# Performance work log

Measured on AMD Instinct MI355X. Metric: run time of the kernel, lower is better.

## Reference

```python
import jax, jax.numpy as jnp
import numpy as np

B, N, C = 4, 4096, 512
C8 = C // 8

def setup_inputs() -> dict:
    key = jax.random.key(0)
    ks = jax.random.split(key, 4)
    x = jax.random.normal(ks[0], (B, N, C), dtype=jnp.float32)
    # 1x1 Conv1D kernels == dense matmuls over channel dim
    Wf = jax.random.normal(ks[1], (C, C8), dtype=jnp.float32) * 0.02
    bf = jnp.zeros((C8,), dtype=jnp.float32)
    Wg = jax.random.normal(ks[2], (C, C8), dtype=jnp.float32) * 0.02
    bg = jnp.zeros((C8,), dtype=jnp.float32)
    Wh = jax.random.normal(ks[3], (C, C), dtype=jnp.float32) * 0.02
    bh = jnp.zeros((C,), dtype=jnp.float32)
    gamma = jnp.float32(1.0)  # learned scalar (zero-init in original; nonzero to exercise path)
    return {"x": x, "Wf": Wf, "bf": bf, "Wg": Wg, "bg": bg, "Wh": Wh, "bh": bh, "gamma": gamma}

def reference(x, Wf, bf, Wg, bg, Wh, bh, gamma):
    # 1x1 conv projections (kernel_size=1 -> per-position matmul)
    f_x = jnp.einsum('bnc,cd->bnd', x, Wf) + bf          # [B, N, C/8]
    g_x = jnp.einsum('bnc,cd->bnd', x, Wg) + bg          # [B, N, C/8]
    h_x = jnp.einsum('bnc,cd->bnd', x, Wh) + bh          # [B, N, C]
    # unscaled single-head attention: softmax(f g^T) h
    scores = jnp.einsum('bnd,bmd->bnm', f_x, g_x)        # [B, N, N]
    attn = jax.nn.softmax(scores, axis=-1)
    out = jnp.einsum('bnm,bmd->bnd', attn, h_x)          # [B, N, C]
    return x + gamma * out
```

## Files before the change

kernel.cpp:

```cpp
#include <hip/hip_runtime.h>
#include <stdint.h>

typedef uint16_t u16;
typedef __attribute__((ext_vector_type(8))) __bf16    bf16x8;
typedef __attribute__((ext_vector_type(4))) __bf16    bf16x4;
typedef __attribute__((ext_vector_type(8))) uint16_t  u16x8;
typedef __attribute__((ext_vector_type(4))) uint16_t  u16x4;
typedef __attribute__((ext_vector_type(4))) float     f32x4;

#define LOG2E 1.44269504088896340736f
#define MFMA16(a, b, c) __builtin_amdgcn_mfma_f32_16x16x32_bf16((a), (b), (c), 0, 0, 0)

__device__ __forceinline__ u16 f2b(float f) {
  uint32_t u = __builtin_bit_cast(uint32_t, f);
  u += 0x7fffu + ((u >> 16) & 1u);
  return (u16)(u >> 16);
}

__device__ __forceinline__ bf16x8 ldsFrag(const u16* base, int row, int chunk) {
  const u16* p = base + row * 64 + ((chunk ^ (row & 7)) << 3);
  u16x8 raw = *(const u16x8*)p;
  return __builtin_bit_cast(bf16x8, raw);
}
__device__ __forceinline__ void ldsPut(u16* base, int row, int logicalChunk, u16x8 v) {
  u16* p = base + row * 64 + ((logicalChunk ^ (row & 7)) << 3);
  *(u16x8*)p = v;
}

__device__ __forceinline__ void dma16(const u16* g, u16* l) {
  __builtin_amdgcn_global_load_lds(
      (const __attribute__((address_space(1))) uint32_t*)g,
      (__attribute__((address_space(3))) uint32_t*)l, 16, 0, 0);
}

__global__ __launch_bounds__(256) void pack_weights2(
    const float* __restrict__ Wf, const float* __restrict__ Wg,
    const float* __restrict__ Wh, const float* __restrict__ bfv,
    const float* __restrict__ bgv, const float* __restrict__ bhv,
    u16* __restrict__ Wt, float* __restrict__ biasc) {
  __shared__ u16 T[64 * 64];
  const int nt = blockIdx.x >> 3;
  const int kt = blockIdx.x & 7;
  const int n0 = nt * 64, k0 = kt * 64;
  const float* src; int stride, cbase; float scale = 1.0f;
  if (nt == 0)      { src = Wf; stride = 64;  cbase = 0;        scale = LOG2E; }
  else if (nt == 1) { src = Wg; stride = 64;  cbase = 0; }
  else              { src = Wh; stride = 512; cbase = n0 - 128; }
  const int t = threadIdx.x;
  const int cl = (t & 15) * 4, r0 = t >> 4;
#pragma unroll
  for (int j = 0; j < 4; ++j) {
    int r = r0 + j * 16;
    f32x4 v = *(const f32x4*)(src + (size_t)(k0 + r) * stride + cbase + cl);
    u16x4 o;
#pragma unroll
    for (int i = 0; i < 4; ++i) o[i] = f2b(v[i] * scale);
    *(u16x4*)(T + r * 64 + cl) = o;
  }
  __syncthreads();
  const int n = t >> 2, kq = (t & 3) * 16;
  u16x8 a, b2;
#pragma unroll
  for (int i = 0; i < 8; ++i) { a[i] = T[(kq + i) * 64 + n]; b2[i] = T[(kq + 8 + i) * 64 + n]; }
  *(u16x8*)(Wt + (size_t)(n0 + n) * 512 + k0 + kq) = a;
  *(u16x8*)(Wt + (size_t)(n0 + n) * 512 + k0 + kq + 8) = b2;
  if (kt == 0 && t < 64) {
    float bv = (nt == 0) ? bfv[t] * LOG2E : (nt == 1) ? bgv[t] : bhv[cbase + t];
    biasc[n0 + t] = bv;
  }
}

__global__ __launch_bounds__(256, 2) void proj_gemm(
    const float* __restrict__ x, const u16* __restrict__ Wt,
    const float* __restrict__ biasc,
    u16* __restrict__ fo, u16* __restrict__ go, u16* __restrict__ ht) {
  __shared__ u16 smem[128 * 128];
  u16* lds_a = smem;
  u16* lds_b = smem + 128 * 64;
  const int t = threadIdx.x, lane = t & 63, wave = t >> 6;
  const int m0 = blockIdx.x * 128, n0 = blockIdx.y * 128;
  const int wr = wave >> 1, wc = wave & 1;
  const int l15 = lane & 15, l4 = lane >> 4;
  const int sr = t >> 3, sc = t & 7;

  f32x4 acc[4][4];
#pragma unroll
  for (int i = 0; i < 4; ++i)
#pragma unroll
    for (int j = 0; j < 4; ++j) acc[i][j] = (f32x4)(0.f);

  for (int kb = 0; kb < 8; ++kb) {
    const int k0 = kb * 64;
    if (kb) __syncthreads();
#pragma unroll
    for (int p = 0; p < 4; ++p) {
      int rr = p * 32 + sr;
      const float* s = x + (size_t)(m0 + rr) * 512 + k0 + sc * 8;
      f32x4 a0 = *(const f32x4*)s;
      f32x4 a1 = *(const f32x4*)(s + 4);
      u16x8 v;
#pragma unroll
      for (int i = 0; i < 4; ++i) { v[i] = f2b(a0[i]); v[4 + i] = f2b(a1[i]); }
      ldsPut(lds_a, rr, sc, v);
    }
#pragma unroll
    for (int p = 0; p < 4; ++p) {
      int rr = p * 32 + sr;
      u16x8 v = *(const u16x8*)(Wt + (size_t)(n0 + rr) * 512 + k0 + sc * 8);
      ldsPut(lds_b, rr, sc, v);
    }
    __syncthreads();
#pragma unroll
    for (int ks = 0; ks < 2; ++ks) {
      const int chunk = ks * 4 + l4;
      bf16x8 af[4], bq[4];
#pragma unroll
      for (int mt = 0; mt < 4; ++mt) af[mt] = ldsFrag(lds_a, wr * 64 + mt * 16 + l15, chunk);
#pragma unroll
      for (int nt = 0; nt < 4; ++nt) bq[nt] = ldsFrag(lds_b, wc * 64 + nt * 16 + l15, chunk);
#pragma unroll
      for (int mt = 0; mt < 4; ++mt)
#pragma unroll
        for (int nt = 0; nt < 4; ++nt) acc[mt][nt] = MFMA16(af[mt], bq[nt], acc[mt][nt]);
    }
  }

  if (n0 >= 128) {
    __syncthreads();
#pragma unroll
    for (int nt = 0; nt < 4; ++nt) {
      int nl = wc * 64 + nt * 16 + l15;
      float bv = biasc[n0 + nl];
#pragma unroll
      for (int mt = 0; mt < 4; ++mt) {
        int mb = wr * 64 + mt * 16 + (l4 << 2);
        f32x4 a = acc[mt][nt];
        u16x4 v;
#pragma unroll
        for (int r = 0; r < 4; ++r) v[r] = f2b(a[r] + bv);
        u16* dst = smem + nl * 128 + (((mb >> 3) ^ (nl & 7)) << 3) + (mb & 7);
        *(u16x4*)dst = v;
      }
    }
    __syncthreads();
    const int bb = m0 >> 12, posb = m0 & 4095;
    const int row0 = t >> 4, c16 = t & 15;
#pragma unroll
    for (int j = 0; j < 8; ++j) {
      int rr = row0 + j * 16;
      u16x8 v = *(const u16x8*)(smem + rr * 128 + ((c16 ^ (rr & 7)) << 3));
      int vcol = n0 - 128 + rr;
      *(u16x8*)(ht + ((size_t)(bb * 512 + vcol) << 12) + posb + c16 * 8) = v;
    }
  } else {
#pragma unroll
    for (int nt = 0; nt < 4; ++nt) {
      int n = wc * 64 + nt * 16 + l15;
      float bv = biasc[n];
#pragma unroll
      for (int mt = 0; mt < 4; ++mt) {
        int mrow = m0 + wr * 64 + mt * 16 + (l4 << 2);
        f32x4 a = acc[mt][nt];
        if (n < 64) {
#pragma unroll
          for (int r = 0; r < 4; ++r) fo[(size_t)(mrow + r) * 64 + n] = f2b(a[r] + bv);
        } else {
#pragma unroll
          for (int r = 0; r < 4; ++r) go[(size_t)(mrow + r) * 64 + (n - 64)] = f2b(a[r] + bv);
        }
      }
    }
  }
}

__global__ __launch_bounds__(256, 4) void attn3(
    const u16* __restrict__ fq, const u16* __restrict__ gk,
    const u16* __restrict__ ht, const float* __restrict__ x,
    const float* __restrict__ gamma_p, float* __restrict__ out) {
  __shared__ u16 lds_g[64 * 64];
  __shared__ u16 lds_p[64 * 64];
  __shared__ float lds_red[4 * 64];
  __shared__ float lds_linv[64];

  const int i = blockIdx.x;
  const int slice = i & 15;
  const int b = slice >> 2, vq = slice & 3;
  const int qb = i >> 4;
  const int q0 = qb * 64, vc0 = vq * 128;

  const int t = threadIdx.x, lane = t & 63, w = t >> 6;
  const int l15 = lane & 15, l4 = lane >> 4;
  const float gamma = gamma_p[0];
  const int dmarow = lane >> 3, dmachunk = (lane & 7) ^ (lane >> 3);

  const u16* gkb = gk + (size_t)(b * 4096) * 64;
  const u16* htw = ht + ((size_t)(b * 512 + vc0 + w * 32)) * 4096;

  bf16x8 fB[4][2];
#pragma unroll
  for (int qt = 0; qt < 4; ++qt)
#pragma unroll
    for (int ks = 0; ks < 2; ++ks) {
      const u16* p = fq + (size_t)(b * 4096 + q0 + qt * 16 + l15) * 64 + ks * 32 + l4 * 8;
      fB[qt][ks] = __builtin_bit_cast(bf16x8, *(const u16x8*)p);
    }

  f32x4 oacc[4][2];
#pragma unroll
  for (int qt = 0; qt < 4; ++qt)
#pragma unroll
    for (int ct = 0; ct < 2; ++ct) oacc[qt][ct] = (f32x4)(0.f);
  float lrun[4] = {0.f, 0.f, 0.f, 0.f};

  auto stage_g = [&](int k0g) {
#pragma unroll
    for (int ii = 0; ii < 2; ++ii) {
      int rw = w * 16 + ii * 8;
      const u16* src = gkb + (size_t)(k0g + rw + dmarow) * 64 + dmachunk * 8;
      dma16(src, lds_g + rw * 64);
    }
  };

  stage_g(0);
  __syncthreads();

  for (int kt = 0; kt < 64; ++kt) {
    const int k0 = kt * 64;
    f32x4 sacc[4];
#pragma unroll
    for (int qt = 0; qt < 4; ++qt) sacc[qt] = (f32x4)(0.f);
#pragma unroll
    for (int ks = 0; ks < 2; ++ks) {
      bf16x8 gA = ldsFrag(lds_g, w * 16 + l15, ks * 4 + l4);
#pragma unroll
      for (int qt = 0; qt < 4; ++qt) sacc[qt] = MFMA16(gA, fB[qt][ks], sacc[qt]);
    }
#pragma unroll
    for (int qt = 0; qt < 4; ++qt) {
      f32x4 s = sacc[qt];
      f32x4 p;
#pragma unroll
      for (int r = 0; r < 4; ++r) p[r] = __builtin_amdgcn_exp2f(s[r]);
      lrun[qt] += (p[0] + p[1]) + (p[2] + p[3]);
      bf16x4 pb;
#pragma unroll
      for (int r = 0; r < 4; ++r) pb[r] = (__bf16)p[r];
      int row = qt * 16 + l15;
      int keyb = w * 16 + (l4 << 2);
      u16* dst = lds_p + row * 64 + (((keyb >> 3) ^ (row & 7)) << 3) + (keyb & 7);
      *(u16x4*)dst = __builtin_bit_cast(u16x4, pb);
    }
    __syncthreads();
    if (kt < 63) stage_g(k0 + 64);
#pragma unroll
    for (int ks = 0; ks < 2; ++ks) {
      bf16x8 hb[2], pf[4];
#pragma unroll
      for (int ct = 0; ct < 2; ++ct) {
        const u16* hp = htw + (size_t)(ct * 16 + l15) * 4096 + k0 + ks * 32 + l4 * 8;
        hb[ct] = __builtin_bit_cast(bf16x8, *(const u16x8*)hp);
      }
#pragma unroll
      for (int qt = 0; qt < 4; ++qt)
        pf[qt] = ldsFrag(lds_p, qt * 16 + l15, ks * 4 + l4);
#pragma unroll
      for (int qt = 0; qt < 4; ++qt)
#pragma unroll
        for (int ct = 0; ct < 2; ++ct)
          oacc[qt][ct] = MFMA16(pf[qt], hb[ct], oacc[qt][ct]);
    }
    __syncthreads();
  }

#pragma unroll
  for (int qt = 0; qt < 4; ++qt) {
    lrun[qt] += __shfl_xor(lrun[qt], 16);
    lrun[qt] += __shfl_xor(lrun[qt], 32);
  }
  if (l4 == 0) {
#pragma unroll
    for (int qt = 0; qt < 4; ++qt) lds_red[w * 64 + qt * 16 + l15] = lrun[qt];
  }
  __syncthreads();
  if (t < 64) {
    float s = (lds_red[t] + lds_red[64 + t]) + (lds_red[128 + t] + lds_red[192 + t]);
    lds_linv[t] = 1.0f / s;
  }
  __syncthreads();

#pragma unroll
  for (int qt = 0; qt < 4; ++qt) {
    f32x4 linv = *(const f32x4*)&lds_linv[qt * 16 + (l4 << 2)];
#pragma unroll
    for (int ct = 0; ct < 2; ++ct) {
      int c = vc0 + w * 32 + ct * 16 + l15;
#pragma unroll
      for (int r = 0; r < 4; ++r) {
        int q = q0 + qt * 16 + (l4 << 2) + r;
        size_t idx = ((size_t)(b * 4096 + q) << 9) + c;
        out[idx] = x[idx] + gamma * oacc[qt][ct][r] * linv[r];
      }
    }
  }
}

extern "C" void kernel_launch(void* const* d_in, const int* in_sizes, int n_in,
                              void* d_out, int out_size, void* d_ws, size_t ws_size,
                              hipStream_t stream) {
  const float* x   = (const float*)d_in[0];
  const float* Wf  = (const float*)d_in[1];
  const float* bfv = (const float*)d_in[2];
  const float* Wg  = (const float*)d_in[3];
  const float* bgv = (const float*)d_in[4];
  const float* Wh  = (const float*)d_in[5];
  const float* bhv = (const float*)d_in[6];
  const float* gam = (const float*)d_in[7];
  float* out = (float*)d_out;

  char* ws = (char*)d_ws;
  u16*   Wt    = (u16*)(ws);
  float* biasc = (float*)(ws + 655360);
  u16*   fo    = (u16*)(ws + 657920);
  u16*   go    = (u16*)(ws + 2755072);
  u16*   ht    = (u16*)(ws + 4852224);

  pack_weights2<<<80, 256, 0, stream>>>(Wf, Wg, Wh, bfv, bgv, bhv, Wt, biasc);
  proj_gemm<<<dim3(128, 5), 256, 0, stream>>>(x, Wt, biasc, fo, go, ht);
  attn3<<<1024, 256, 0, stream>>>(fo, go, ht, x, gam, out);
}
```

Measured before the change: 255.5 us.

## Restructure attention kernel to 2 waves with 32x32 MFMA and per-wave query rows

The attention kernel moves from four waves sharing a 64-query tile with 16x16 MFMAs to two waves, each owning 32 query rows and all 128 value channels, using 32x32x16 MFMAs. Each wave keeps its P tile in a private LDS region, so the cross-wave barrier between the softmax write and the PV product goes away, leaving one barrier per iteration. The G tile is double-buffered so the next tile's DMA is issued before the current tile's compute. In exchange, each wave loads more H data per step and holds larger accumulators, and the smaller blocks mean fewer waves per block, which may hurt latency hiding.

```diff
diff --git a/kernel.cpp b/kernel.cpp
--- a/kernel.cpp
+++ b/kernel.cpp
@@ -2,14 +2,16 @@
 #include <stdint.h>
 
 typedef uint16_t u16;
-typedef __attribute__((ext_vector_type(8))) __bf16    bf16x8;
-typedef __attribute__((ext_vector_type(4))) __bf16    bf16x4;
-typedef __attribute__((ext_vector_type(8))) uint16_t  u16x8;
-typedef __attribute__((ext_vector_type(4))) uint16_t  u16x4;
-typedef __attribute__((ext_vector_type(4))) float     f32x4;
+typedef __attribute__((ext_vector_type(8)))  __bf16    bf16x8;
+typedef __attribute__((ext_vector_type(4)))  __bf16    bf16x4;
+typedef __attribute__((ext_vector_type(8)))  uint16_t  u16x8;
+typedef __attribute__((ext_vector_type(4)))  uint16_t  u16x4;
+typedef __attribute__((ext_vector_type(4)))  float     f32x4;
+typedef __attribute__((ext_vector_type(16))) float     f32x16;
 
 #define LOG2E 1.44269504088896340736f
 #define MFMA16(a, b, c) __builtin_amdgcn_mfma_f32_16x16x32_bf16((a), (b), (c), 0, 0, 0)
+#define MFMA32(a, b, c) __builtin_amdgcn_mfma_f32_32x32x16_bf16((a), (b), (c), 0, 0, 0)
 
 __device__ __forceinline__ u16 f2b(float f) {
   uint32_t u = __builtin_bit_cast(uint32_t, f);
@@ -173,14 +175,13 @@
   }
 }
 
-__global__ __launch_bounds__(256, 4) void attn3(
+__global__ __launch_bounds__(128, 2) void attn5(
     const u16* __restrict__ fq, const u16* __restrict__ gk,
     const u16* __restrict__ ht, const float* __restrict__ x,
     const float* __restrict__ gamma_p, float* __restrict__ out) {
-  __shared__ u16 lds_g[64 * 64];
-  __shared__ u16 lds_p[64 * 64];
-  __shared__ float lds_red[4 * 64];
-  __shared__ float lds_linv[64];
+  __shared__ u16 lds_g[2][64 * 64];
+  __shared__ u16 lds_p[2][32 * 64];
+  __shared__ float lds_linv[2][32];
 
   const int i = blockIdx.x;
   const int slice = i & 15;
@@ -189,117 +190,105 @@
   const int q0 = qb * 64, vc0 = vq * 128;
 
   const int t = threadIdx.x, lane = t & 63, w = t >> 6;
-  const int l15 = lane & 15, l4 = lane >> 4;
+  const int l31 = lane & 31, hi = lane >> 5;
   const float gamma = gamma_p[0];
   const int dmarow = lane >> 3, dmachunk = (lane & 7) ^ (lane >> 3);
 
   const u16* gkb = gk + (size_t)(b * 4096) * 64;
-  const u16* htw = ht + ((size_t)(b * 512 + vc0 + w * 32)) * 4096;
-
-  bf16x8 fB[4][2];
-#pragma unroll
-  for (int qt = 0; qt < 4; ++qt)
-#pragma unroll
-    for (int ks = 0; ks < 2; ++ks) {
-      const u16* p = fq + (size_t)(b * 4096 + q0 + qt * 16 + l15) * 64 + ks * 32 + l4 * 8;
-      fB[qt][ks] = __builtin_bit_cast(bf16x8, *(const u16x8*)p);
-    }
-
-  f32x4 oacc[4][2];
-#pragma unroll
-  for (int qt = 0; qt < 4; ++qt)
-#pragma unroll
-    for (int ct = 0; ct < 2; ++ct) oacc[qt][ct] = (f32x4)(0.f);
-  float lrun[4] = {0.f, 0.f, 0.f, 0.f};
-
-  auto stage_g = [&](int k0g) {
-#pragma unroll
-    for (int ii = 0; ii < 2; ++ii) {
-      int rw = w * 16 + ii * 8;
-      const u16* src = gkb + (size_t)(k0g + rw + dmarow) * 64 + dmachunk * 8;
-      dma16(src, lds_g + rw * 64);
+  const u16* htw = ht + (size_t)(b * 512 + vc0) * 4096;
+  u16* ldsp = lds_p[w];
+
+  bf16x8 fB[4];
+  {
+    const u16* fb = fq + (size_t)(b * 4096 + q0 + w * 32 + l31) * 64 + hi * 8;
+#pragma unroll
+    for (int s = 0; s < 4; ++s)
+      fB[s] = __builtin_bit_cast(bf16x8, *(const u16x8*)(fb + s * 16));
+  }
+
+  f32x16 oacc[4];
+#pragma unroll
+  for (int ct = 0; ct < 4; ++ct) oacc[ct] = (f32x16)(0.f);
+  float lrun = 0.f;
+
+  auto stage_g = [&](int k0g, u16* dst) {
+#pragma unroll
+    for (int ii = 0; ii < 4; ++ii) {
+      int rw = w * 32 + ii * 8;
+      dma16(gkb + (size_t)(k0g + rw + dmarow) * 64 + dmachunk * 8, dst + rw * 64);
     }
   };
 
-  stage_g(0);
+  stage_g(0, lds_g[0]);
   __syncthreads();
 
   for (int kt = 0; kt < 64; ++kt) {
     const int k0 = kt * 64;
-    f32x4 sacc[4];
-#pragma unroll
-    for (int qt = 0; qt < 4; ++qt) sacc[qt] = (f32x4)(0.f);
-#pragma unroll
-    for (int ks = 0; ks < 2; ++ks) {
-      bf16x8 gA = ldsFrag(lds_g, w * 16 + l15, ks * 4 + l4);
-#pragma unroll
-      for (int qt = 0; qt < 4; ++qt) sacc[qt] = MFMA16(gA, fB[qt][ks], sacc[qt]);
-    }
-#pragma unroll
-    for (int qt = 0; qt < 4; ++qt) {
-      f32x4 s = sacc[qt];
-      f32x4 p;
-#pragma unroll
-      for (int r = 0; r < 4; ++r) p[r] = __builtin_amdgcn_exp2f(s[r]);
-      lrun[qt] += (p[0] + p[1]) + (p[2] + p[3]);
-      bf16x4 pb;
-#pragma unroll
-      for (int r = 0; r < 4; ++r) pb[r] = (__bf16)p[r];
-      int row = qt * 16 + l15;
-      int keyb = w * 16 + (l4 << 2);
-      u16* dst = lds_p + row * 64 + (((keyb >> 3) ^ (row & 7)) << 3) + (keyb & 7);
-      *(u16x4*)dst = __builtin_bit_cast(u16x4, pb);
+    const u16* gbuf = lds_g[kt & 1];
+    if (kt < 63) stage_g(k0 + 64, lds_g[(kt & 1) ^ 1]);
+
+    f32x16 sac[2];
+#pragma unroll
+    for (int kg = 0; kg < 2; ++kg) {
+      f32x16 s = (f32x16)(0.f);
+#pragma unroll
+      for (int ss = 0; ss < 4; ++ss) {
+        bf16x8 gA = ldsFrag(gbuf, kg * 32 + l31, ss * 2 + hi);
+        s = MFMA32(gA, fB[ss], s);
+      }
+      sac[kg] = s;
+    }
+
+#pragma unroll
+    for (int kg = 0; kg < 2; ++kg) {
+      u16x8 hbr[2][4];
+#pragma unroll
+      for (int h = 0; h < 2; ++h)
+#pragma unroll
+        for (int ct = 0; ct < 4; ++ct)
+          hbr[h][ct] = *(const u16x8*)(htw + (size_t)(ct * 32 + l31) * 4096 +
+                                       k0 + kg * 32 + h * 16 + hi * 8);
+      f32x16 p;
+#pragma unroll
+      for (int r = 0; r < 16; ++r) p[r] = __builtin_amdgcn_exp2f(sac[kg][r]);
+      lrun += ((p[0] + p[1]) + (p[2] + p[3])) + ((p[4] + p[5]) + (p[6] + p[7])) +
+              ((p[8] + p[9]) + (p[10] + p[11])) + ((p[12] + p[13]) + (p[14] + p[15]));
+#pragma unroll
+      for (int Q = 0; Q < 4; ++Q) {
+        bf16x4 pb;
+#pragma unroll
+        for (int r = 0; r < 4; ++r) pb[r] = (__bf16)p[4 * Q + r];
+        int chunk = kg * 4 + Q;
+        u16* dst = ldsp + l31 * 64 + ((chunk ^ (l31 & 7)) << 3) + 4 * hi;
+        *(u16x4*)dst = __builtin_bit_cast(u16x4, pb);
+      }
+#pragma unroll
+      for (int h = 0; h < 2; ++h) {
+        bf16x8 pa = ldsFrag(ldsp, l31, kg * 4 + h * 2 + hi);
+#pragma unroll
+        for (int ct = 0; ct < 4; ++ct)
+          oacc[ct] = MFMA32(pa, __builtin_bit_cast(bf16x8, hbr[h][ct]), oacc[ct]);
+      }
     }
     __syncthreads();
-    if (kt < 63) stage_g(k0 + 64);
-#pragma unroll
-    for (int ks = 0; ks < 2; ++ks) {
-      bf16x8 hb[2], pf[4];
-#pragma unroll
-      for (int ct = 0; ct < 2; ++ct) {
-        const u16* hp = htw + (size_t)(ct * 16 + l15) * 4096 + k0 + ks * 32 + l4 * 8;
-        hb[ct] = __builtin_bit_cast(bf16x8, *(const u16x8*)hp);
-      }
-#pragma unroll
-      for (int qt = 0; qt < 4; ++qt)
-        pf[qt] = ldsFrag(lds_p, qt * 16 + l15, ks * 4 + l4);
-#pragma unroll
-      for (int qt = 0; qt < 4; ++qt)
-#pragma unroll
-        for (int ct = 0; ct < 2; ++ct)
-          oacc[qt][ct] = MFMA16(pf[qt], hb[ct], oacc[qt][ct]);
-    }
-    __syncthreads();
-  }
-
-#pragma unroll
-  for (int qt = 0; qt < 4; ++qt) {
-    lrun[qt] += __shfl_xor(lrun[qt], 16);
-    lrun[qt] += __shfl_xor(lrun[qt], 32);
-  }
-  if (l4 == 0) {
-#pragma unroll
-    for (int qt = 0; qt < 4; ++qt) lds_red[w * 64 + qt * 16 + l15] = lrun[qt];
-  }
+  }
+
+  lrun += __shfl_xor(lrun, 32);
+  if (lane < 32) lds_linv[w][l31] = 1.0f / lrun;
   __syncthreads();
-  if (t < 64) {
-    float s = (lds_red[t] + lds_red[64 + t]) + (lds_red[128 + t] + lds_red[192 + t]);
-    lds_linv[t] = 1.0f / s;
-  }
-  __syncthreads();
-
-#pragma unroll
-  for (int qt = 0; qt < 4; ++qt) {
-    f32x4 linv = *(const f32x4*)&lds_linv[qt * 16 + (l4 << 2)];
-#pragma unroll
-    for (int ct = 0; ct < 2; ++ct) {
-      int c = vc0 + w * 32 + ct * 16 + l15;
-#pragma unroll
-      for (int r = 0; r < 4; ++r) {
-        int q = q0 + qt * 16 + (l4 << 2) + r;
-        size_t idx = ((size_t)(b * 4096 + q) << 9) + c;
-        out[idx] = x[idx] + gamma * oacc[qt][ct][r] * linv[r];
-      }
+  float linvv[16];
+#pragma unroll
+  for (int r = 0; r < 16; ++r)
+    linvv[r] = lds_linv[w][(r & 3) + 8 * (r >> 2) + 4 * hi];
+
+#pragma unroll
+  for (int ct = 0; ct < 4; ++ct) {
+    int c = vc0 + ct * 32 + l31;
+#pragma unroll
+    for (int r = 0; r < 16; ++r) {
+      int q = q0 + w * 32 + (r & 3) + 8 * (r >> 2) + 4 * hi;
+      size_t idx = ((size_t)(b * 4096 + q) << 9) + c;
+      out[idx] = x[idx] + gamma * oacc[ct][r] * linvv[r];
     }
   }
 }
@@ -326,5 +315,5 @@
 
   pack_weights2<<<80, 256, 0, stream>>>(Wf, Wg, Wh, bfv, bgv, bhv, Wt, biasc);
   proj_gemm<<<dim3(128, 5), 256, 0, stream>>>(x, Wt, biasc, fo, go, ht);
-  attn3<<<1024, 256, 0, stream>>>(fo, go, ht, x, gam, out);
-}
+  attn5<<<1024, 128, 0, stream>>>(fo, go, ht, x, gam, out);
+}
```

After: 354.9 us. +38.9%, slower.

## Pre-convert x to bf16 and load GEMM tiles via direct global-to-LDS DMA

Applied to the files above, without the earlier changes.

Adds a separate kernel that converts x from fp32 to bf16 once, rather than having each of the 5 column-block GEMM workgroups convert it again. The projection GEMM then fills its A and B tiles with global_load_lds 16-byte DMA, using swizzled chunk addressing that matches the LDS XOR layout, instead of staging through registers. The aim is to cut redundant fp32 reads, conversion ALU work and register traffic in the GEMM. In exchange it adds a kernel launch plus an extra bf16 write and read of x (16 MB).

```diff
diff --git a/kernel.cpp b/kernel.cpp
--- a/kernel.cpp
+++ b/kernel.cpp
@@ -2,11 +2,11 @@
 #include <stdint.h>
 
 typedef uint16_t u16;
-typedef __attribute__((ext_vector_type(8))) __bf16    bf16x8;
-typedef __attribute__((ext_vector_type(4))) __bf16    bf16x4;
-typedef __attribute__((ext_vector_type(8))) uint16_t  u16x8;
-typedef __attribute__((ext_vector_type(4))) uint16_t  u16x4;
-typedef __attribute__((ext_vector_type(4))) float     f32x4;
+typedef __attribute__((ext_vector_type(8)))  __bf16    bf16x8;
+typedef __attribute__((ext_vector_type(4)))  __bf16    bf16x4;
+typedef __attribute__((ext_vector_type(8)))  uint16_t  u16x8;
+typedef __attribute__((ext_vector_type(4)))  uint16_t  u16x4;
+typedef __attribute__((ext_vector_type(4)))  float     f32x4;
 
 #define LOG2E 1.44269504088896340736f
 #define MFMA16(a, b, c) __builtin_amdgcn_mfma_f32_16x16x32_bf16((a), (b), (c), 0, 0, 0)
@@ -31,6 +31,17 @@
   __builtin_amdgcn_global_load_lds(
       (const __attribute__((address_space(1))) uint32_t*)g,
       (__attribute__((address_space(3))) uint32_t*)l, 16, 0, 0);
+}
+
+__global__ __launch_bounds__(256) void xconv(
+    const float* __restrict__ x, u16* __restrict__ xb) {
+  size_t idx = ((size_t)blockIdx.x * 256 + threadIdx.x) * 8;
+  f32x4 a0 = *(const f32x4*)(x + idx);
+  f32x4 a1 = *(const f32x4*)(x + idx + 4);
+  u16x8 v;
+#pragma unroll
+  for (int i = 0; i < 4; ++i) { v[i] = f2b(a0[i]); v[4 + i] = f2b(a1[i]); }
+  *(u16x8*)(xb + idx) = v;
 }
 
 __global__ __launch_bounds__(256) void pack_weights2(
@@ -71,7 +82,7 @@
 }
 
 __global__ __launch_bounds__(256, 2) void proj_gemm(
-    const float* __restrict__ x, const u16* __restrict__ Wt,
+    const u16* __restrict__ xb, const u16* __restrict__ Wt,
     const float* __restrict__ biasc,
     u16* __restrict__ fo, u16* __restrict__ go, u16* __restrict__ ht) {
   __shared__ u16 smem[128 * 128];
@@ -81,7 +92,7 @@
   const int m0 = blockIdx.x * 128, n0 = blockIdx.y * 128;
   const int wr = wave >> 1, wc = wave & 1;
   const int l15 = lane & 15, l4 = lane >> 4;
-  const int sr = t >> 3, sc = t & 7;
+  const int dmarow = lane >> 3, dmachunk = (lane & 7) ^ (lane >> 3);
 
   f32x4 acc[4][4];
 #pragma unroll
@@ -93,21 +104,16 @@
     const int k0 = kb * 64;
     if (kb) __syncthreads();
 #pragma unroll
-    for (int p = 0; p < 4; ++p) {
-      int rr = p * 32 + sr;
-      const float* s = x + (size_t)(m0 + rr) * 512 + k0 + sc * 8;
-      f32x4 a0 = *(const f32x4*)s;
-      f32x4 a1 = *(const f32x4*)(s + 4);
-      u16x8 v;
-#pragma unroll
-      for (int i = 0; i < 4; ++i) { v[i] = f2b(a0[i]); v[4 + i] = f2b(a1[i]); }
-      ldsPut(lds_a, rr, sc, v);
-    }
-#pragma unroll
-    for (int p = 0; p < 4; ++p) {
-      int rr = p * 32 + sr;
-      u16x8 v = *(const u16x8*)(Wt + (size_t)(n0 + rr) * 512 + k0 + sc * 8);
-      ldsPut(lds_b, rr, sc, v);
+    for (int ii = 0; ii < 4; ++ii) {
+      int rw = wave * 32 + ii * 8;
+      dma16(xb + (size_t)(m0 + rw + dmarow) * 512 + k0 + dmachunk * 8,
+            lds_a + rw * 64);
+    }
+#pragma unroll
+    for (int ii = 0; ii < 4; ++ii) {
+      int rw = wave * 32 + ii * 8;
+      dma16(Wt + (size_t)(n0 + rw + dmarow) * 512 + k0 + dmachunk * 8,
+            lds_b + rw * 64);
     }
     __syncthreads();
 #pragma unroll
@@ -323,8 +329,10 @@
   u16*   fo    = (u16*)(ws + 657920);
   u16*   go    = (u16*)(ws + 2755072);
   u16*   ht    = (u16*)(ws + 4852224);
-
+  u16*   xb    = (u16*)(ws + 21629440);
+
+  xconv<<<4096, 256, 0, stream>>>(x, xb);
   pack_weights2<<<80, 256, 0, stream>>>(Wf, Wg, Wh, bfv, bgv, bhv, Wt, biasc);
-  proj_gemm<<<dim3(128, 5), 256, 0, stream>>>(x, Wt, biasc, fo, go, ht);
+  proj_gemm<<<dim3(128, 5), 256, 0, stream>>>(xb, Wt, biasc, fo, go, ht);
   attn3<<<1024, 256, 0, stream>>>(fo, go, ht, x, gam, out);
 }
```

Result: faster. 248.7 us (-2.7%).
